# Performance work log

Hardware: AMD Instinct MI355X
Metric: run time of the kernel (lower is better)

The kernel has to match this reference:

```python
import jax, jax.numpy as jnp
import numpy as np

N, E, F_IN, HID, HEADS, CLS = 50000, 600000, 128, 128, 4, 10
OUT_PER_HEAD = HID // HEADS  # 32
NEG_SLOPE = 0.2
BN_EPS = 1e-5


def _gat_conv(h, src, dst, W, att_src, att_dst, bias, heads, out_dim, concat, num_nodes):
    # h: [N, in]; W: [in, heads*out]; att_*: [heads, out]; src/dst include self-loops
    hp = (h @ W).reshape(num_nodes, heads, out_dim)          # [N, H, D]
    a_s = jnp.sum(hp * att_src[None], axis=-1)               # [N, H]
    a_d = jnp.sum(hp * att_dst[None], axis=-1)               # [N, H]
    alpha = jax.nn.leaky_relu(a_s[src] + a_d[dst], NEG_SLOPE)  # [E, H]
    m = jax.ops.segment_max(alpha, dst, num_segments=num_nodes)
    m = jnp.where(jnp.isfinite(m), m, 0.0)
    ex = jnp.exp(alpha - m[dst])
    denom = jax.ops.segment_sum(ex, dst, num_segments=num_nodes)
    attn = ex / (denom[dst] + 1e-16)                         # segment softmax over dst
    msg = hp[src] * attn[..., None]                          # [E, H, D]
    out = jax.ops.segment_sum(msg, dst, num_segments=num_nodes)  # [N, H, D]
    out = out.reshape(num_nodes, heads * out_dim) if concat else out.mean(axis=1)
    return out + bias


def _bn_eval(x, gamma, beta):
    # eval-mode BatchNorm1d with running_mean=0, running_var=1
    return x * (gamma / jnp.sqrt(1.0 + BN_EPS)) + beta


def setup_inputs() -> dict:
    key = jax.random.key(0)
    ks = jax.random.split(key, 16)
    x = jax.random.normal(ks[0], (N, F_IN), dtype=jnp.float32)
    edge_index = jax.random.randint(ks[1], (2, E), 0, N, dtype=jnp.int64)
    s = 0.1
    return {
        "x": x,
        "edge_index": edge_index,
        "W0": jax.random.normal(ks[2], (F_IN, HID), jnp.float32) * s,
        "as0": jax.random.normal(ks[3], (HEADS, OUT_PER_HEAD), jnp.float32) * s,
        "ad0": jax.random.normal(ks[4], (HEADS, OUT_PER_HEAD), jnp.float32) * s,
        "b0": jnp.zeros((HID,), jnp.float32),
        "g0": jnp.ones((HID,), jnp.float32),
        "be0": jnp.zeros((HID,), jnp.float32),
        "W1": jax.random.normal(ks[5], (HID, HID), jnp.float32) * s,
        "as1": jax.random.normal(ks[6], (HEADS, OUT_PER_HEAD), jnp.float32) * s,
        "ad1": jax.random.normal(ks[7], (HEADS, OUT_PER_HEAD), jnp.float32) * s,
        "b1": jnp.zeros((HID,), jnp.float32),
        "g1": jnp.ones((HID,), jnp.float32),
        "be1": jnp.zeros((HID,), jnp.float32),
        "W2": jax.random.normal(ks[8], (HID, CLS), jnp.float32) * s,
        "as2": jax.random.normal(ks[9], (1, CLS), jnp.float32) * s,
        "ad2": jax.random.normal(ks[10], (1, CLS), jnp.float32) * s,
        "b2": jnp.zeros((CLS,), jnp.float32),
    }


def reference(x, edge_index, W0, as0, ad0, b0, g0, be0,
              W1, as1, ad1, b1, g1, be1, W2, as2, ad2, b2):
    # add self-loops (PyG GATConv default)
    loop = jnp.arange(N, dtype=edge_index.dtype)
    src = jnp.concatenate([edge_index[0], loop])
    dst = jnp.concatenate([edge_index[1], loop])
    h = _gat_conv(x, src, dst, W0, as0, ad0, b0, HEADS, OUT_PER_HEAD, True, N)
    h = jax.nn.elu(_bn_eval(h, g0, be0))
    h = _gat_conv(h, src, dst, W1, as1, ad1, b1, HEADS, OUT_PER_HEAD, True, N)
    h = jax.nn.elu(_bn_eval(h, g1, be1))
    out = _gat_conv(h, src, dst, W2, as2, ad2, b2, 1, CLS, False, N)
    return out
```

## Files before the change

### kernel.cpp

```cpp
#include <hip/hip_runtime.h>
#include <hip/hip_bf16.h>
#include <hip/hip_fp16.h>
#include <math.h>

#define N_NODES 50000
#define N_EDGES 600000
#define E_TOT   (N_EDGES + N_NODES)
#define F       128
#define HEADS   4
#define DHEAD   32
#define CLS     10
#define CLS_PAD 16


__global__ void count_deg(const int* __restrict__ ei, int* __restrict__ deg) {
    int e = blockIdx.x * blockDim.x + threadIdx.x;
    if (e >= N_EDGES) return;
    atomicAdd(&deg[ei[N_EDGES + e]], 1);
}

#define SCAN_BLOCK 256
#define SCAN_ITEMS 4

__global__ void scan1(const int* __restrict__ deg, int* __restrict__ ptr,
                      int* __restrict__ blockSums, int n) {
    __shared__ int sdata[SCAN_BLOCK];
    int t = threadIdx.x;
    int base = blockIdx.x * (SCAN_BLOCK * SCAN_ITEMS) + t * SCAN_ITEMS;
    int v[SCAN_ITEMS];
    int sum = 0;
    #pragma unroll
    for (int i = 0; i < SCAN_ITEMS; i++) {
        int idx = base + i;
        v[i] = (idx < n) ? (deg[idx] + 1) : 0;
        sum += v[i];
    }
    sdata[t] = sum;
    __syncthreads();
    for (int off = 1; off < SCAN_BLOCK; off <<= 1) {
        int x = 0;
        if (t >= off) x = sdata[t - off];
        __syncthreads();
        if (t >= off) sdata[t] += x;
        __syncthreads();
    }
    int excl = (t > 0) ? sdata[t - 1] : 0;
    if (t == SCAN_BLOCK - 1) blockSums[blockIdx.x] = sdata[t];
    int run = excl;
    #pragma unroll
    for (int i = 0; i < SCAN_ITEMS; i++) {
        int idx = base + i;
        if (idx < n) ptr[idx] = run;
        run += v[i];
    }
}

__global__ void scan2(int* __restrict__ blockSums, int nb) {
    if (threadIdx.x == 0 && blockIdx.x == 0) {
        int run = 0;
        for (int i = 0; i < nb; i++) { int v = blockSums[i]; blockSums[i] = run; run += v; }
    }
}

__global__ void scan3(int* __restrict__ ptr, const int* __restrict__ blockSums,
                      int* __restrict__ cursor, int* __restrict__ csr, int n, int total) {
    int i = blockIdx.x * blockDim.x + threadIdx.x;
    if (i < n) {
        int v = ptr[i] + blockSums[i / (SCAN_BLOCK * SCAN_ITEMS)];
        ptr[i] = v;
        cursor[i] = v + 1;
        csr[v] = i;
    }
    if (i == 0) ptr[n] = total;
}

__global__ void scatter_edges(const int* __restrict__ ei, int* __restrict__ cursor,
                              int* __restrict__ csr_src) {
    int e = blockIdx.x * blockDim.x + threadIdx.x;
    if (e >= N_EDGES) return;
    int s = ei[e], d = ei[N_EDGES + e];
    int pos = atomicAdd(&cursor[d], 1);
    csr_src[pos] = s;
}


__global__ __launch_bounds__(256) void conv_w(const float* __restrict__ W0,
                                              const float* __restrict__ W1,
                                              __half* __restrict__ Wt0,
                                              __half* __restrict__ Wt1) {
    int idx = blockIdx.x * 256 + threadIdx.x;
    if (idx >= 128 * 128) return;
    int k = idx >> 7, c = idx & 127;
    int e = k ^ ((c & 7) << 3);
    Wt0[c * 128 + e] = __float2half(W0[idx]);
    Wt1[c * 128 + e] = __float2half(W1[idx]);
}


using half8_t  = __attribute__((ext_vector_type(8))) _Float16;
using floatx4  = __attribute__((ext_vector_type(4))) float;

template<bool HALF_IN>
__global__ __launch_bounds__(256) void gemm_att_mfma(const void* __restrict__ Ain,
                                                     const __half* __restrict__ Wt,
                                                     const float* __restrict__ att_s,
                                                     const float* __restrict__ att_d,
                                                     __half* __restrict__ C,
                                                     float* __restrict__ a_s,
                                                     float* __restrict__ a_d, int nrows) {
    __shared__ _Float16 As[64 * 128];
    __shared__ _Float16 Ws[128 * 128];
    int t = threadIdx.x;
    int row0 = blockIdx.x * 64;

    #pragma unroll
    for (int idx = t; idx < 128 * 128 / 8; idx += 256)
        ((float4*)Ws)[idx] = ((const float4*)Wt)[idx];

    if constexpr (HALF_IN) {
        const __half* A = (const __half*)Ain;
        #pragma unroll
        for (int idx = t; idx < 64 * 16; idx += 256) {
            int r = idx >> 4, g = idx & 15;
            float4 v = make_float4(0.f, 0.f, 0.f, 0.f);
            if (row0 + r < nrows)
                v = *(const float4*)(A + (size_t)(row0 + r) * 128 + g * 8);
            int gs = g ^ (r & 7);
            *(float4*)&As[r * 128 + (gs << 3)] = v;
        }
    } else {
        const float* A = (const float*)Ain;
        #pragma unroll
        for (int idx = t; idx < 64 * 16; idx += 256) {
            int r = idx >> 4, g = idx & 15;
            float4 v0 = make_float4(0.f, 0.f, 0.f, 0.f), v1 = v0;
            if (row0 + r < nrows) {
                const float4* p = (const float4*)(A + (size_t)(row0 + r) * 128 + g * 8);
                v0 = p[0]; v1 = p[1];
            }
            int gs = g ^ (r & 7);
            union { _Float16 h[8]; float4 f; } u;
            u.h[0] = (_Float16)v0.x; u.h[1] = (_Float16)v0.y;
            u.h[2] = (_Float16)v0.z; u.h[3] = (_Float16)v0.w;
            u.h[4] = (_Float16)v1.x; u.h[5] = (_Float16)v1.y;
            u.h[6] = (_Float16)v1.z; u.h[7] = (_Float16)v1.w;
            *(float4*)&As[r * 128 + (gs << 3)] = u.f;
        }
    }
    __syncthreads();

    int wave = t >> 6, l = t & 63;
    int lr = l & 15, lg = l >> 4;
    int arow = wave * 16 + lr;

    floatx4 acc[8];
    #pragma unroll
    for (int c2 = 0; c2 < 8; c2++) acc[c2] = (floatx4){0.f, 0.f, 0.f, 0.f};

    #pragma unroll
    for (int ks = 0; ks < 4; ks++) {
        int gk = ks * 4 + lg;
        half8_t af = *(const half8_t*)&As[arow * 128 + ((gk ^ (arow & 7)) << 3)];
        #pragma unroll
        for (int c2 = 0; c2 < 8; c2++) {
            int col = c2 * 16 + lr;
            half8_t bf = *(const half8_t*)&Ws[col * 128 + ((gk ^ (col & 7)) << 3)];
            acc[c2] = __builtin_amdgcn_mfma_f32_16x16x32_f16(bf, af, acc[c2], 0, 0, 0);
        }
    }

    int row = row0 + arow;
    bool rowOk = row < nrows;

    #pragma unroll
    for (int c2 = 0; c2 < 8; c2++) {
        __half2 p0 = __floats2half2_rn(acc[c2][0], acc[c2][1]);
        __half2 p1 = __floats2half2_rn(acc[c2][2], acc[c2][3]);
        uint2 u;
        u.x = *(unsigned*)&p0;
        u.y = *(unsigned*)&p1;
        if (rowOk) ((uint2*)C)[(size_t)row * 32 + c2 * 4 + lg] = u;
    }

    float ps[4] = {0.f, 0.f, 0.f, 0.f}, pd[4] = {0.f, 0.f, 0.f, 0.f};
    #pragma unroll
    for (int c2 = 0; c2 < 8; c2++) {
        #pragma unroll
        for (int r = 0; r < 4; r++) {
            int col = c2 * 16 + lg * 4 + r;
            float v = acc[c2][r];
            ps[c2 >> 1] += v * att_s[col];
            pd[c2 >> 1] += v * att_d[col];
        }
    }
    #pragma unroll
    for (int hh = 0; hh < 4; hh++) {
        ps[hh] += __shfl_xor(ps[hh], 16); ps[hh] += __shfl_xor(ps[hh], 32);
        pd[hh] += __shfl_xor(pd[hh], 16); pd[hh] += __shfl_xor(pd[hh], 32);
    }
    if (lg == 0 && rowOk) {
        *(float4*)(a_s + (size_t)row * 4) = make_float4(ps[0], ps[1], ps[2], ps[3]);
        *(float4*)(a_d + (size_t)row * 4) = make_float4(pd[0], pd[1], pd[2], pd[3]);
    }
}


__global__ __launch_bounds__(128) void gat_aggr(const __half2* __restrict__ hp,
                                                const float* __restrict__ a_s,
                                                const float* __restrict__ a_d,
                                                const int* __restrict__ ptr,
                                                const int* __restrict__ csr,
                                                const float* __restrict__ bias,
                                                const float* __restrict__ gamma,
                                                const float* __restrict__ beta,
                                                __half2* __restrict__ out) {
    int t = threadIdx.x;
    int node = __builtin_amdgcn_readfirstlane(blockIdx.x * 2 + (t >> 6));
    int local = t & 63;
    int h = local >> 4;
    int beg = ptr[node], end = ptr[node + 1];
    float adh = a_d[(size_t)node * 4 + h];
    float ax = 0.f, ay = 0.f, l = 0.f;
    int i = beg;
    for (; i + 3 < end; i += 4) {
        int s0 = csr[i], s1 = csr[i + 1], s2 = csr[i + 2], s3 = csr[i + 3];
        float al0 = a_s[(size_t)s0 * 4 + h] + adh;
        float al1 = a_s[(size_t)s1 * 4 + h] + adh;
        float al2 = a_s[(size_t)s2 * 4 + h] + adh;
        float al3 = a_s[(size_t)s3 * 4 + h] + adh;
        al0 = (al0 > 0.f) ? al0 : 0.2f * al0;
        al1 = (al1 > 0.f) ? al1 : 0.2f * al1;
        al2 = (al2 > 0.f) ? al2 : 0.2f * al2;
        al3 = (al3 > 0.f) ? al3 : 0.2f * al3;
        float w0 = __expf(al0), w1 = __expf(al1), w2 = __expf(al2), w3 = __expf(al3);
        float2 v0 = __half22float2(hp[(size_t)s0 * 64 + local]);
        float2 v1 = __half22float2(hp[(size_t)s1 * 64 + local]);
        float2 v2 = __half22float2(hp[(size_t)s2 * 64 + local]);
        float2 v3 = __half22float2(hp[(size_t)s3 * 64 + local]);
        l  += w0 + w1 + w2 + w3;
        ax += w0 * v0.x + w1 * v1.x + w2 * v2.x + w3 * v3.x;
        ay += w0 * v0.y + w1 * v1.y + w2 * v2.y + w3 * v3.y;
    }
    for (; i < end; i++) {
        int s0 = csr[i];
        float al = a_s[(size_t)s0 * 4 + h] + adh;
        al = (al > 0.f) ? al : 0.2f * al;
        float w = __expf(al);
        float2 v = __half22float2(hp[(size_t)s0 * 64 + local]);
        l  += w;
        ax += w * v.x;
        ay += w * v.y;
    }
    float inv = 1.f / (l + 1e-16f);
    int c = local * 2;
    const float rs = rsqrtf(1.f + 1e-5f);
    float2 bs = *(const float2*)(bias + c);
    float2 gm = *(const float2*)(gamma + c);
    float2 bt = *(const float2*)(beta + c);
    float vx = ax * inv + bs.x;
    float vy = ay * inv + bs.y;
    vx = vx * (gm.x * rs) + bt.x;
    vy = vy * (gm.y * rs) + bt.y;
    vx = (vx > 0.f) ? vx : expm1f(vx);
    vy = (vy > 0.f) ? vy : expm1f(vy);
    out[(size_t)node * 64 + local] = __floats2half2_rn(vx, vy);
}


__global__ __launch_bounds__(256) void cls_fused(const __half* __restrict__ A,
                                                 const float* __restrict__ W2,
                                                 const float* __restrict__ as2,
                                                 const float* __restrict__ ad2,
                                                 float* __restrict__ hp2,
                                                 float* __restrict__ asn,
                                                 float* __restrict__ adn) {
    __shared__ float W2s[128 * CLS];
    __shared__ float av[2 * CLS];
    int t = threadIdx.x;
    for (int idx = t; idx < 128 * CLS; idx += 256) W2s[idx] = W2[idx];
    if (t < CLS) av[t] = as2[t];
    else if (t < 2 * CLS) av[t] = ad2[t - CLS];
    __syncthreads();

    int node = blockIdx.x * 64 + (t >> 2);
    int q = t & 3;
    if (node >= N_NODES) return;
    float acc[CLS];
    #pragma unroll
    for (int c = 0; c < CLS; c++) acc[c] = 0.f;
    const float4* arow = (const float4*)(A + (size_t)node * 128 + q * 32);
    #pragma unroll
    for (int kk = 0; kk < 4; kk++) {
        float4 raw = arow[kk];
        __half2* hh = (__half2*)&raw;
        #pragma unroll
        for (int j = 0; j < 4; j++) {
            float2 f = __half22float2(hh[j]);
            int k = q * 32 + kk * 8 + j * 2;
            #pragma unroll
            for (int c = 0; c < CLS; c++)
                acc[c] += f.x * W2s[k * CLS + c] + f.y * W2s[(k + 1) * CLS + c];
        }
    }
    #pragma unroll
    for (int c = 0; c < CLS; c++) {
        acc[c] += __shfl_xor(acc[c], 1, 4);
        acc[c] += __shfl_xor(acc[c], 2, 4);
    }
    if (q == 0) {
        float s = 0.f, d = 0.f;
        float* row = hp2 + (size_t)node * CLS_PAD;
        #pragma unroll
        for (int c = 0; c < CLS; c++) {
            row[c] = acc[c];
            s += acc[c] * av[c];
            d += acc[c] * av[CLS + c];
        }
        asn[node] = s;
        adn[node] = d;
    }
}

__global__ __launch_bounds__(256) void gat_aggr2(const float* __restrict__ hp2,
                                                 const float* __restrict__ asn,
                                                 const float* __restrict__ adn,
                                                 const int* __restrict__ ptr,
                                                 const int* __restrict__ csr,
                                                 const float* __restrict__ b2,
                                                 float* __restrict__ out) {
    int gid = blockIdx.x * blockDim.x + threadIdx.x;
    int node = gid >> 4;
    int c = gid & 15;
    if (node >= N_NODES) return;
    int beg = ptr[node], end = ptr[node + 1];
    int cc = (c < CLS) ? c : 0;
    float adv = adn[node];
    float acc = 0.f, l = 0.f;
    int i = beg;
    for (; i + 3 < end; i += 4) {
        int s0 = csr[i], s1 = csr[i + 1], s2 = csr[i + 2], s3 = csr[i + 3];
        float al0 = asn[s0] + adv;
        float al1 = asn[s1] + adv;
        float al2 = asn[s2] + adv;
        float al3 = asn[s3] + adv;
        al0 = (al0 > 0.f) ? al0 : 0.2f * al0;
        al1 = (al1 > 0.f) ? al1 : 0.2f * al1;
        al2 = (al2 > 0.f) ? al2 : 0.2f * al2;
        al3 = (al3 > 0.f) ? al3 : 0.2f * al3;
        float w0 = __expf(al0), w1 = __expf(al1), w2 = __expf(al2), w3 = __expf(al3);
        float v0 = hp2[(size_t)s0 * CLS_PAD + cc];
        float v1 = hp2[(size_t)s1 * CLS_PAD + cc];
        float v2 = hp2[(size_t)s2 * CLS_PAD + cc];
        float v3 = hp2[(size_t)s3 * CLS_PAD + cc];
        l   += w0 + w1 + w2 + w3;
        acc += w0 * v0 + w1 * v1 + w2 * v2 + w3 * v3;
    }
    for (; i < end; i++) {
        int s0 = csr[i];
        float al = asn[s0] + adv;
        al = (al > 0.f) ? al : 0.2f * al;
        float w = __expf(al);
        l += w;
        acc += w * hp2[(size_t)s0 * CLS_PAD + cc];
    }
    if (c < CLS) out[(size_t)node * CLS + c] = acc / (l + 1e-16f) + b2[c];
}


extern "C" void kernel_launch(void* const* d_in, const int* in_sizes, int n_in,
                              void* d_out, int out_size, void* d_ws, size_t ws_size,
                              hipStream_t stream) {
    const float* x   = (const float*)d_in[0];
    const int*   ei  = (const int*)  d_in[1];
    const float* W0  = (const float*)d_in[2];
    const float* as0 = (const float*)d_in[3];
    const float* ad0 = (const float*)d_in[4];
    const float* b0  = (const float*)d_in[5];
    const float* g0  = (const float*)d_in[6];
    const float* be0 = (const float*)d_in[7];
    const float* W1  = (const float*)d_in[8];
    const float* as1 = (const float*)d_in[9];
    const float* ad1 = (const float*)d_in[10];
    const float* b1  = (const float*)d_in[11];
    const float* g1  = (const float*)d_in[12];
    const float* be1 = (const float*)d_in[13];
    const float* W2  = (const float*)d_in[14];
    const float* as2 = (const float*)d_in[15];
    const float* ad2 = (const float*)d_in[16];
    const float* b2  = (const float*)d_in[17];

    char* ws = (char*)d_ws;
    size_t off = 0;
    auto alloc = [&](size_t bytes) -> void* {
        void* p = ws + off;
        off += (bytes + 255) & ~(size_t)255;
        return p;
    };
    int*    ptr    = (int*)   alloc((N_NODES + 1) * sizeof(int));
    int*    cursor = (int*)   alloc(N_NODES * sizeof(int));
    int*    bsums  = (int*)   alloc(64 * sizeof(int));
    int*    csr    = (int*)   alloc(E_TOT * sizeof(int));
    __half* hp     = (__half*)alloc((size_t)N_NODES * 128 * sizeof(__half));
    __half* hc     = (__half*)alloc((size_t)N_NODES * 128 * sizeof(__half));
    float*  a_s    = (float*) alloc(N_NODES * 4 * sizeof(float));
    float*  a_d    = (float*) alloc(N_NODES * 4 * sizeof(float));
    float*  hp2    = (float*) alloc((size_t)N_NODES * CLS_PAD * sizeof(float));
    float*  asn    = (float*) alloc(N_NODES * sizeof(float));
    float*  adn    = (float*) alloc(N_NODES * sizeof(float));
    __half* Wt0    = (__half*)alloc(128 * 128 * sizeof(__half));
    __half* Wt1    = (__half*)alloc(128 * 128 * sizeof(__half));

    hipMemsetAsync(cursor, 0, N_NODES * sizeof(int), stream);
    count_deg<<<(N_EDGES + 255) / 256, 256, 0, stream>>>(ei, cursor);
    int nScanBlocks = (N_NODES + SCAN_BLOCK * SCAN_ITEMS - 1) / (SCAN_BLOCK * SCAN_ITEMS);
    scan1<<<nScanBlocks, SCAN_BLOCK, 0, stream>>>(cursor, ptr, bsums, N_NODES);
    scan2<<<1, 64, 0, stream>>>(bsums, nScanBlocks);
    scan3<<<(N_NODES + 255) / 256, 256, 0, stream>>>(ptr, bsums, cursor, csr, N_NODES, E_TOT);
    scatter_edges<<<(N_EDGES + 255) / 256, 256, 0, stream>>>(ei, cursor, csr);

    conv_w<<<64, 256, 0, stream>>>(W0, W1, Wt0, Wt1);

    int gemmBlocks = (N_NODES + 63) / 64;

    gemm_att_mfma<false><<<gemmBlocks, 256, 0, stream>>>(x, Wt0, as0, ad0, hp, a_s, a_d, N_NODES);
    gat_aggr<<<N_NODES / 2, 128, 0, stream>>>((const __half2*)hp, a_s, a_d, ptr, csr,
                                              b0, g0, be0, (__half2*)hc);

    gemm_att_mfma<true><<<gemmBlocks, 256, 0, stream>>>(hc, Wt1, as1, ad1, hp, a_s, a_d, N_NODES);
    gat_aggr<<<N_NODES / 2, 128, 0, stream>>>((const __half2*)hp, a_s, a_d, ptr, csr,
                                              b1, g1, be1, (__half2*)hc);

    cls_fused<<<(N_NODES + 63) / 64, 256, 0, stream>>>(hc, W2, as2, ad2, hp2, asn, adn);
    gat_aggr2<<<(N_NODES * 16 + 255) / 256, 256, 0, stream>>>(hp2, asn, adn, ptr, csr, b2,
                                                              (float*)d_out);
}
```

Baseline: 298.8 us.

## Software-pipeline gather loads in GAT aggregation and split edges across lane groups

The layer-1/2 aggregation kernel now prefetches the next four neighbours' indices, attention scores and features while it computes the current batch. The tail loop is replaced by clamped indices with zeroed weights, so every iteration does the same work. The final-layer aggregation now gives each node a full wavefront, with four 16-lane groups handling different edges in parallel and a shuffle reduction at the end. Index arithmetic is also narrowed from size_t to int. The prefetch raises register pressure, and the final layer's tail iterations do some wasted work.

```diff
diff --git a/kernel.cpp b/kernel.cpp
--- a/kernel.cpp
+++ b/kernel.cpp
@@ -124,7 +124,7 @@
             int r = idx >> 4, g = idx & 15;
             float4 v = make_float4(0.f, 0.f, 0.f, 0.f);
             if (row0 + r < nrows)
-                v = *(const float4*)(A + (size_t)(row0 + r) * 128 + g * 8);
+                v = *(const float4*)(A + (row0 + r) * 128 + g * 8);
             int gs = g ^ (r & 7);
             *(float4*)&As[r * 128 + (gs << 3)] = v;
         }
@@ -135,7 +135,7 @@
             int r = idx >> 4, g = idx & 15;
             float4 v0 = make_float4(0.f, 0.f, 0.f, 0.f), v1 = v0;
             if (row0 + r < nrows) {
-                const float4* p = (const float4*)(A + (size_t)(row0 + r) * 128 + g * 8);
+                const float4* p = (const float4*)(A + (row0 + r) * 128 + g * 8);
                 v0 = p[0]; v1 = p[1];
             }
             int gs = g ^ (r & 7);
@@ -179,7 +179,7 @@
         uint2 u;
         u.x = *(unsigned*)&p0;
         u.y = *(unsigned*)&p1;
-        if (rowOk) ((uint2*)C)[(size_t)row * 32 + c2 * 4 + lg] = u;
+        if (rowOk) ((uint2*)C)[row * 32 + c2 * 4 + lg] = u;
     }
 
     float ps[4] = {0.f, 0.f, 0.f, 0.f}, pd[4] = {0.f, 0.f, 0.f, 0.f};
@@ -199,8 +199,8 @@
         pd[hh] += __shfl_xor(pd[hh], 16); pd[hh] += __shfl_xor(pd[hh], 32);
     }
     if (lg == 0 && rowOk) {
-        *(float4*)(a_s + (size_t)row * 4) = make_float4(ps[0], ps[1], ps[2], ps[3]);
-        *(float4*)(a_d + (size_t)row * 4) = make_float4(pd[0], pd[1], pd[2], pd[3]);
+        *(float4*)(a_s + row * 4) = make_float4(ps[0], ps[1], ps[2], ps[3]);
+        *(float4*)(a_d + row * 4) = make_float4(pd[0], pd[1], pd[2], pd[3]);
     }
 }
 
@@ -219,38 +219,57 @@
     int local = t & 63;
     int h = local >> 4;
     int beg = ptr[node], end = ptr[node + 1];
-    float adh = a_d[(size_t)node * 4 + h];
+    float adh = a_d[node * 4 + h];
     float ax = 0.f, ay = 0.f, l = 0.f;
+
     int i = beg;
-    for (; i + 3 < end; i += 4) {
-        int s0 = csr[i], s1 = csr[i + 1], s2 = csr[i + 2], s3 = csr[i + 3];
-        float al0 = a_s[(size_t)s0 * 4 + h] + adh;
-        float al1 = a_s[(size_t)s1 * 4 + h] + adh;
-        float al2 = a_s[(size_t)s2 * 4 + h] + adh;
-        float al3 = a_s[(size_t)s3 * 4 + h] + adh;
-        al0 = (al0 > 0.f) ? al0 : 0.2f * al0;
-        al1 = (al1 > 0.f) ? al1 : 0.2f * al1;
-        al2 = (al2 > 0.f) ? al2 : 0.2f * al2;
-        al3 = (al3 > 0.f) ? al3 : 0.2f * al3;
-        float w0 = __expf(al0), w1 = __expf(al1), w2 = __expf(al2), w3 = __expf(al3);
-        float2 v0 = __half22float2(hp[(size_t)s0 * 64 + local]);
-        float2 v1 = __half22float2(hp[(size_t)s1 * 64 + local]);
-        float2 v2 = __half22float2(hp[(size_t)s2 * 64 + local]);
-        float2 v3 = __half22float2(hp[(size_t)s3 * 64 + local]);
+    int e1 = (i + 1 < end) ? i + 1 : beg;
+    int e2 = (i + 2 < end) ? i + 2 : beg;
+    int e3 = (i + 3 < end) ? i + 3 : beg;
+    int cs0 = csr[i], cs1 = csr[e1], cs2 = csr[e2], cs3 = csr[e3];
+    float ca0 = a_s[cs0 * 4 + h], ca1 = a_s[cs1 * 4 + h];
+    float ca2 = a_s[cs2 * 4 + h], ca3 = a_s[cs3 * 4 + h];
+    __half2 ch0 = hp[cs0 * 64 + local], ch1 = hp[cs1 * 64 + local];
+    __half2 ch2 = hp[cs2 * 64 + local], ch3 = hp[cs3 * 64 + local];
+
+    while (true) {
+        int inext = i + 4;
+        bool more = inext < end;
+        int ns0, ns1, ns2, ns3;
+        float na0, na1, na2, na3;
+        __half2 nh0, nh1, nh2, nh3;
+        if (more) {
+            int f1 = (inext + 1 < end) ? inext + 1 : beg;
+            int f2 = (inext + 2 < end) ? inext + 2 : beg;
+            int f3 = (inext + 3 < end) ? inext + 3 : beg;
+            ns0 = csr[inext]; ns1 = csr[f1]; ns2 = csr[f2]; ns3 = csr[f3];
+            na0 = a_s[ns0 * 4 + h]; na1 = a_s[ns1 * 4 + h];
+            na2 = a_s[ns2 * 4 + h]; na3 = a_s[ns3 * 4 + h];
+            nh0 = hp[ns0 * 64 + local]; nh1 = hp[ns1 * 64 + local];
+            nh2 = hp[ns2 * 64 + local]; nh3 = hp[ns3 * 64 + local];
+        }
+        float al0 = ca0 + adh; al0 = (al0 > 0.f) ? al0 : 0.2f * al0;
+        float al1 = ca1 + adh; al1 = (al1 > 0.f) ? al1 : 0.2f * al1;
+        float al2 = ca2 + adh; al2 = (al2 > 0.f) ? al2 : 0.2f * al2;
+        float al3 = ca3 + adh; al3 = (al3 > 0.f) ? al3 : 0.2f * al3;
+        float w0 = __expf(al0);
+        float w1 = (i + 1 < end) ? __expf(al1) : 0.f;
+        float w2 = (i + 2 < end) ? __expf(al2) : 0.f;
+        float w3 = (i + 3 < end) ? __expf(al3) : 0.f;
+        float2 v0 = __half22float2(ch0);
+        float2 v1 = __half22float2(ch1);
+        float2 v2 = __half22float2(ch2);
+        float2 v3 = __half22float2(ch3);
         l  += w0 + w1 + w2 + w3;
         ax += w0 * v0.x + w1 * v1.x + w2 * v2.x + w3 * v3.x;
         ay += w0 * v0.y + w1 * v1.y + w2 * v2.y + w3 * v3.y;
-    }
-    for (; i < end; i++) {
-        int s0 = csr[i];
-        float al = a_s[(size_t)s0 * 4 + h] + adh;
-        al = (al > 0.f) ? al : 0.2f * al;
-        float w = __expf(al);
-        float2 v = __half22float2(hp[(size_t)s0 * 64 + local]);
-        l  += w;
-        ax += w * v.x;
-        ay += w * v.y;
-    }
+        if (!more) break;
+        i = inext;
+        cs0 = ns0; cs1 = ns1; cs2 = ns2; cs3 = ns3;
+        ca0 = na0; ca1 = na1; ca2 = na2; ca3 = na3;
+        ch0 = nh0; ch1 = nh1; ch2 = nh2; ch3 = nh3;
+    }
+
     float inv = 1.f / (l + 1e-16f);
     int c = local * 2;
     const float rs = rsqrtf(1.f + 1e-5f);
@@ -263,7 +282,7 @@
     vy = vy * (gm.y * rs) + bt.y;
     vx = (vx > 0.f) ? vx : expm1f(vx);
     vy = (vy > 0.f) ? vy : expm1f(vy);
-    out[(size_t)node * 64 + local] = __floats2half2_rn(vx, vy);
+    out[node * 64 + local] = __floats2half2_rn(vx, vy);
 }
 
 
@@ -288,7 +307,7 @@
     float acc[CLS];
     #pragma unroll
     for (int c = 0; c < CLS; c++) acc[c] = 0.f;
-    const float4* arow = (const float4*)(A + (size_t)node * 128 + q * 32);
+    const float4* arow = (const float4*)(A + node * 128 + q * 32);
     #pragma unroll
     for (int kk = 0; kk < 4; kk++) {
         float4 raw = arow[kk];
@@ -309,7 +328,7 @@
     }
     if (q == 0) {
         float s = 0.f, d = 0.f;
-        float* row = hp2 + (size_t)node * CLS_PAD;
+        float* row = hp2 + node * CLS_PAD;
         #pragma unroll
         for (int c = 0; c < CLS; c++) {
             row[c] = acc[c];
@@ -320,6 +339,7 @@
         adn[node] = d;
     }
 }
+
 
 __global__ __launch_bounds__(256) void gat_aggr2(const float* __restrict__ hp2,
                                                  const float* __restrict__ asn,
@@ -328,42 +348,32 @@
                                                  const int* __restrict__ csr,
                                                  const float* __restrict__ b2,
                                                  float* __restrict__ out) {
-    int gid = blockIdx.x * blockDim.x + threadIdx.x;
-    int node = gid >> 4;
-    int c = gid & 15;
-    if (node >= N_NODES) return;
+    int t = threadIdx.x;
+    int node = __builtin_amdgcn_readfirstlane(blockIdx.x * 4 + (t >> 6));
+    int lane = t & 63;
+    int g = lane >> 4;
+    int c = lane & 15;
     int beg = ptr[node], end = ptr[node + 1];
-    int cc = (c < CLS) ? c : 0;
     float adv = adn[node];
     float acc = 0.f, l = 0.f;
-    int i = beg;
-    for (; i + 3 < end; i += 4) {
-        int s0 = csr[i], s1 = csr[i + 1], s2 = csr[i + 2], s3 = csr[i + 3];
-        float al0 = asn[s0] + adv;
-        float al1 = asn[s1] + adv;
-        float al2 = asn[s2] + adv;
-        float al3 = asn[s3] + adv;
-        al0 = (al0 > 0.f) ? al0 : 0.2f * al0;
-        al1 = (al1 > 0.f) ? al1 : 0.2f * al1;
-        al2 = (al2 > 0.f) ? al2 : 0.2f * al2;
-        al3 = (al3 > 0.f) ? al3 : 0.2f * al3;
-        float w0 = __expf(al0), w1 = __expf(al1), w2 = __expf(al2), w3 = __expf(al3);
-        float v0 = hp2[(size_t)s0 * CLS_PAD + cc];
-        float v1 = hp2[(size_t)s1 * CLS_PAD + cc];
-        float v2 = hp2[(size_t)s2 * CLS_PAD + cc];
-        float v3 = hp2[(size_t)s3 * CLS_PAD + cc];
-        l   += w0 + w1 + w2 + w3;
-        acc += w0 * v0 + w1 * v1 + w2 * v2 + w3 * v3;
-    }
-    for (; i < end; i++) {
-        int s0 = csr[i];
-        float al = asn[s0] + adv;
+    for (int i = beg; i < end; i += 4) {
+        int e1 = (i + 1 < end) ? i + 1 : beg;
+        int e2 = (i + 2 < end) ? i + 2 : beg;
+        int e3 = (i + 3 < end) ? i + 3 : beg;
+        int s0 = csr[i], s1 = csr[e1], s2 = csr[e2], s3 = csr[e3];
+        int s = (g == 0) ? s0 : (g == 1) ? s1 : (g == 2) ? s2 : s3;
+        float a = asn[s];
+        float al = a + adv;
         al = (al > 0.f) ? al : 0.2f * al;
-        float w = __expf(al);
-        l += w;
-        acc += w * hp2[(size_t)s0 * CLS_PAD + cc];
-    }
-    if (c < CLS) out[(size_t)node * CLS + c] = acc / (l + 1e-16f) + b2[c];
+        float w = (i + g < end) ? __expf(al) : 0.f;
+        float v = hp2[s * CLS_PAD + c];
+        l   += w;
+        acc += w * v;
+    }
+    acc += __shfl_xor(acc, 16); acc += __shfl_xor(acc, 32);
+    l   += __shfl_xor(l, 16);   l   += __shfl_xor(l, 32);
+    if (g == 0 && c < CLS)
+        out[node * CLS + c] = acc / (l + 1e-16f) + b2[c];
 }
 
 
@@ -431,6 +441,5 @@
                                               b1, g1, be1, (__half2*)hc);
 
     cls_fused<<<(N_NODES + 63) / 64, 256, 0, stream>>>(hc, W2, as2, ad2, hp2, asn, adn);
-    gat_aggr2<<<(N_NODES * 16 + 255) / 256, 256, 0, stream>>>(hp2, asn, adn, ptr, csr, b2,
-                                                              (float*)d_out);
-}
+    gat_aggr2<<<N_NODES / 4, 256, 0, stream>>>(hp2, asn, adn, ptr, csr, b2, (float*)d_out);
+}
```

Result: slower. 320.2 us (+7.2%).
